# Kernel tuning notes

Hardware: AMD Instinct MI355X
Metric: run time of the kernel (lower is better)

Reference implementation:

```python
import jax, jax.numpy as jnp
import numpy as np

N = 262144   # number of occupied voxels (sparse points)
C = 64       # channels
G = 128
K = 27       # 3x3x3 kernel offsets


def _build_kernel_map(rng):
    # Unique occupied voxel coordinates on a G^3 grid.
    flat = rng.choice(G ** 3, size=N, replace=False)
    order = np.argsort(flat)
    skeys = flat[order]
    coords = np.stack(np.unravel_index(flat, (G, G, G)), axis=1).astype(np.int64)  # [N,3]
    offsets = np.array([[dx, dy, dz] for dx in (-1, 0, 1) for dy in (-1, 0, 1) for dz in (-1, 0, 1)], np.int64)
    nb = np.full((N, K), -1, np.int32)  # -1 == no neighbor at this offset
    for k in range(K):
        nc = coords + offsets[k]
        valid = np.all((nc >= 0) & (nc < G), axis=1)
        nkey = (nc[:, 0] * G + nc[:, 1]) * G + nc[:, 2]
        pos = np.clip(np.searchsorted(skeys, nkey), 0, N - 1)
        hit = valid & (skeys[pos] == nkey)
        nb[hit, k] = order[pos[hit]].astype(np.int32)
    return nb


def setup_inputs() -> dict:
    nb = _build_kernel_map(np.random.default_rng(0))
    key = jax.random.key(0)
    k1, k2, k3, k4, k5 = jax.random.split(key, 5)
    feat = jax.random.normal(k1, (N, C), jnp.float32)
    W = jax.random.normal(k2, (C, C), jnp.float32) / np.float32(np.sqrt(C))   # 1x1 bottleneck weight
    b1 = jax.random.normal(k3, (C,), jnp.float32) * 0.01                      # bottleneck bias
    dw = jax.random.normal(k4, (K, C), jnp.float32) / np.float32(np.sqrt(K))  # channelwise 3^3 kernel
    b2 = jax.random.normal(k5, (C,), jnp.float32) * 0.01                      # channelwise bias
    return {"feat": feat, "neighbor_idx": jnp.asarray(nb), "W": W, "b1": b1, "b2": b2, "dw": dw}


def reference(feat, neighbor_idx, W, b1, b2, dw):
    # bottleneck: 1x1 sparse conv == pointwise linear over features
    bx = feat @ W + b1  # [N,C]
    mask = neighbor_idx >= 0
    safe = jnp.where(mask, neighbor_idx, 0)
    # channelwise (depthwise) 3x3x3 sparse conv: sum over 27 offsets of
    # gathered neighbor features times per-channel weight. scan over the
    # fixed 27 offsets to avoid a [N,27,C] intermediate.
    def body(acc, inp):
        wk, idxk, mk = inp  # [C], [N], [N]
        g = jnp.where(mk[:, None], bx[idxk], 0.0)
        return acc + g * wk, None
    acc, _ = jax.lax.scan(body, jnp.zeros_like(bx), (dw, safe.T, mask.T))
    # residual add (note: the module never applies its ReLU in forward)
    return feat + acc + b2
```

## Files before the change

### kernel.cpp

```cpp
#include <hip/hip_runtime.h>
#include <hip/hip_bf16.h>

#define NPTS 262144
#define NC 64
#define NK 27

typedef __attribute__((ext_vector_type(8))) short bf16x8;
typedef __attribute__((ext_vector_type(4))) float f32x4;

__device__ __forceinline__ unsigned bfr(float x) {
    unsigned u = __float_as_uint(x);
    return (u + 0x7fffu + ((u >> 16) & 1u)) >> 16;
}
__device__ __forceinline__ float bflo(unsigned u) { return __uint_as_float(u << 16); }
__device__ __forceinline__ float bfhi(unsigned u) { return __uint_as_float(u & 0xffff0000u); }

__device__ __forceinline__ unsigned cvtpk(float lo, float hi) {
    unsigned r;
    asm("v_cvt_pk_bf16_f32 %0, %1, %2" : "=v"(r) : "v"(lo), "v"(hi));
    return r;
}

union BF { unsigned u[4]; bf16x8 v; };

__global__ __launch_bounds__(256) void gemm_mfma(const float* __restrict__ feat,
                                                 const float* __restrict__ W,
                                                 const float* __restrict__ b1,
                                                 ushort* __restrict__ bx) {
    __shared__ float Ws[NC * NC];
    __shared__ float b1S[NC];
    int t = threadIdx.x;
#pragma unroll
    for (int i = 0; i < 4; ++i)
        ((float4*)Ws)[t + i * 256] = ((const float4*)W)[t + i * 256];
    if (t < NC) b1S[t] = b1[t];
    __syncthreads();

    int lane = t & 63;
    int col = lane & 15;
    int kg = lane >> 4;
    int wid = blockIdx.x * 4 + (t >> 6);
    const int NWAVES = 1024 * 4;
    const int NTILES = NPTS / 16;

    BF Bf[2][4];
#pragma unroll
    for (int ks = 0; ks < 2; ++ks)
#pragma unroll
        for (int ct = 0; ct < 4; ++ct)
#pragma unroll
            for (int r = 0; r < 4; ++r) {
                float lo = Ws[(ks * 32 + kg * 8 + 2 * r) * NC + ct * 16 + col];
                float hi = Ws[(ks * 32 + kg * 8 + 2 * r + 1) * NC + ct * 16 + col];
                Bf[ks][ct].u[r] = cvtpk(lo, hi);
            }
    float bias[4];
#pragma unroll
    for (int ct = 0; ct < 4; ++ct) bias[ct] = b1S[ct * 16 + col];

    for (int tile = wid; tile < NTILES; tile += NWAVES) {
        long r0 = (long)tile * 16;
        const float* ap = feat + (r0 + col) * NC + kg * 8;
        float4 a0 = *(const float4*)(ap);
        float4 a1 = *(const float4*)(ap + 4);
        float4 a2 = *(const float4*)(ap + 32);
        float4 a3 = *(const float4*)(ap + 36);
        BF A0, A1;
        A0.u[0] = cvtpk(a0.x, a0.y); A0.u[1] = cvtpk(a0.z, a0.w);
        A0.u[2] = cvtpk(a1.x, a1.y); A0.u[3] = cvtpk(a1.z, a1.w);
        A1.u[0] = cvtpk(a2.x, a2.y); A1.u[1] = cvtpk(a2.z, a2.w);
        A1.u[2] = cvtpk(a3.x, a3.y); A1.u[3] = cvtpk(a3.z, a3.w);

        f32x4 acc[4];
#pragma unroll
        for (int ct = 0; ct < 4; ++ct) {
            acc[ct] = (f32x4){bias[ct], bias[ct], bias[ct], bias[ct]};
            acc[ct] = __builtin_amdgcn_mfma_f32_16x16x32_bf16(A0.v, Bf[0][ct].v, acc[ct], 0, 0, 0);
            acc[ct] = __builtin_amdgcn_mfma_f32_16x16x32_bf16(A1.v, Bf[1][ct].v, acc[ct], 0, 0, 0);
        }

        ushort* op = bx + (r0 + kg * 4) * NC + col;
#pragma unroll
        for (int i = 0; i < 4; ++i)
#pragma unroll
            for (int ct = 0; ct < 4; ++ct)
                op[i * NC + ct * 16] = (ushort)bfr(acc[ct][i]);
    }
}

__global__ __launch_bounds__(256) void dwconv(const float* __restrict__ feat,
                                              const int* __restrict__ nb,
                                              const float* __restrict__ b2,
                                              const float* __restrict__ dw,
                                              const ushort* __restrict__ bx,
                                              float* __restrict__ out) {
    __shared__ float dwS[NK * NC];
    __shared__ float b2S[NC];
    int t = threadIdx.x;
    for (int i = t; i < NK * NC; i += 256) dwS[i] = dw[i];
    if (t < NC) b2S[t] = b2[t];
    __syncthreads();

    int b = blockIdx.x;
    int chunk = gridDim.x >> 3;
    int sb = (b & 7) * chunk + (b >> 3);

    long row = (long)sb * 32 + (t >> 3);
    int c0 = (t & 7) * 8;

    const int* nrow = nb + row * NK;
    int idx[NK];
#pragma unroll
    for (int k = 0; k < NK; ++k) idx[k] = nrow[k];

    const float* fp = feat + row * NC + c0;
    float4 fa = *(const float4*)fp;
    float4 fb = *(const float4*)(fp + 4);

    float acc0 = 0.f, acc1 = 0.f, acc2 = 0.f, acc3 = 0.f;
    float acc4 = 0.f, acc5 = 0.f, acc6 = 0.f, acc7 = 0.f;

#pragma unroll
    for (int k = 0; k < NK; ++k) {
        int id = idx[k];
        bool v = id >= 0;
        if (__any(v)) {
            int ids = v ? id : 0;
            uint4 g = *(const uint4*)(bx + (size_t)ids * NC + c0);
            if (!v) { g.x = 0u; g.y = 0u; g.z = 0u; g.w = 0u; }
            float4 w0 = *(const float4*)(dwS + k * NC + c0);
            float4 w1 = *(const float4*)(dwS + k * NC + c0 + 4);
            acc0 += bflo(g.x) * w0.x;
            acc1 += bfhi(g.x) * w0.y;
            acc2 += bflo(g.y) * w0.z;
            acc3 += bfhi(g.y) * w0.w;
            acc4 += bflo(g.z) * w1.x;
            acc5 += bfhi(g.z) * w1.y;
            acc6 += bflo(g.w) * w1.z;
            acc7 += bfhi(g.w) * w1.w;
        }
    }

    float* op = out + row * NC + c0;
    *(float4*)op = make_float4(acc0 + fa.x + b2S[c0 + 0],
                               acc1 + fa.y + b2S[c0 + 1],
                               acc2 + fa.z + b2S[c0 + 2],
                               acc3 + fa.w + b2S[c0 + 3]);
    *(float4*)(op + 4) = make_float4(acc4 + fb.x + b2S[c0 + 4],
                                     acc5 + fb.y + b2S[c0 + 5],
                                     acc6 + fb.z + b2S[c0 + 6],
                                     acc7 + fb.w + b2S[c0 + 7]);
}

extern "C" void kernel_launch(void* const* d_in, const int* in_sizes, int n_in,
                              void* d_out, int out_size, void* d_ws, size_t ws_size,
                              hipStream_t stream) {
    const float* feat = (const float*)d_in[0];
    const int*   nb   = (const int*)d_in[1];
    const float* W    = (const float*)d_in[2];
    const float* b1   = (const float*)d_in[3];
    const float* b2   = (const float*)d_in[4];
    const float* dw   = (const float*)d_in[5];
    float* out = (float*)d_out;
    ushort* bx = (ushort*)d_ws;

    gemm_mfma<<<1024, 256, 0, stream>>>(feat, W, b1, bx);
    dwconv<<<NPTS / 32, 256, 0, stream>>>(feat, nb, b2, dw, bx, out);
}
```

Before: 211.9 us.

## Pack bx stores as bf16 pairs with interleaved channel layout, batch neighbor gathers

The GEMM epilogue now writes bf16 pairs with a single cvt_pk instruction and 32-bit stores, interleaving channel c and c+16 in the bx workspace. The dwconv weights are permuted in shared memory to match this layout, and outputs are de-interleaved. The neighbor-index tile is staged cooperatively into shared memory. Gathers are issued in batches of 9 with the wave-level any-skip removed, so more loads are in flight at once. The cost is higher register pressure.

```diff
diff --git a/kernel.cpp b/kernel.cpp
--- a/kernel.cpp
+++ b/kernel.cpp
@@ -8,10 +8,6 @@
 typedef __attribute__((ext_vector_type(8))) short bf16x8;
 typedef __attribute__((ext_vector_type(4))) float f32x4;
 
-__device__ __forceinline__ unsigned bfr(float x) {
-    unsigned u = __float_as_uint(x);
-    return (u + 0x7fffu + ((u >> 16) & 1u)) >> 16;
-}
 __device__ __forceinline__ float bflo(unsigned u) { return __uint_as_float(u << 16); }
 __device__ __forceinline__ float bfhi(unsigned u) { return __uint_as_float(u & 0xffff0000u); }
 
@@ -22,6 +18,7 @@
 }
 
 union BF { unsigned u[4]; bf16x8 v; };
+
 
 __global__ __launch_bounds__(256) void gemm_mfma(const float* __restrict__ feat,
                                                  const float* __restrict__ W,
@@ -79,12 +76,12 @@
             acc[ct] = __builtin_amdgcn_mfma_f32_16x16x32_bf16(A1.v, Bf[1][ct].v, acc[ct], 0, 0, 0);
         }
 
-        ushort* op = bx + (r0 + kg * 4) * NC + col;
 #pragma unroll
-        for (int i = 0; i < 4; ++i)
-#pragma unroll
-            for (int ct = 0; ct < 4; ++ct)
-                op[i * NC + ct * 16] = (ushort)bfr(acc[ct][i]);
+        for (int i = 0; i < 4; ++i) {
+            uint* bu = (uint*)(bx + (r0 + kg * 4 + i) * NC);
+            bu[col]      = cvtpk(acc[0][i], acc[1][i]);
+            bu[16 + col] = cvtpk(acc[2][i], acc[3][i]);
+        }
     }
 }
 
@@ -96,60 +93,75 @@
                                               float* __restrict__ out) {
     __shared__ float dwS[NK * NC];
     __shared__ float b2S[NC];
+    __shared__ int nbS[32 * NK];
     int t = threadIdx.x;
-    for (int i = t; i < NK * NC; i += 256) dwS[i] = dw[i];
+    for (int i = t; i < NK * NC; i += 256) {
+        int p = i & 63;
+        int ch = ((p >> 1) & 15) + ((p & 1) << 4) + (p & 32);
+        dwS[i] = dw[(i & ~63) + ch];
+    }
     if (t < NC) b2S[t] = b2[t];
-    __syncthreads();
 
     int b = blockIdx.x;
     int chunk = gridDim.x >> 3;
     int sb = (b & 7) * chunk + (b >> 3);
 
-    long row = (long)sb * 32 + (t >> 3);
-    int c0 = (t & 7) * 8;
+    const uint4* nbsrc = (const uint4*)(nb + (size_t)sb * 32 * NK);
+    if (t < 216) ((uint4*)nbS)[t] = nbsrc[t];
+    __syncthreads();
 
-    const int* nrow = nb + row * NK;
-    int idx[NK];
+    int r = t >> 3;
+    int q = t & 7;
+    long row = (long)sb * 32 + r;
+    int lo_c0 = (q < 4) ? 4 * q : 16 + 4 * q;
+    int hi_c0 = lo_c0 + 16;
+
+    float4 flo = *(const float4*)(feat + row * NC + lo_c0);
+    float4 fhi = *(const float4*)(feat + row * NC + hi_c0);
+
+    float acc[8] = {0.f, 0.f, 0.f, 0.f, 0.f, 0.f, 0.f, 0.f};
+
+    const int* nrow = nbS + r * NK;
 #pragma unroll
-    for (int k = 0; k < NK; ++k) idx[k] = nrow[k];
-
-    const float* fp = feat + row * NC + c0;
-    float4 fa = *(const float4*)fp;
-    float4 fb = *(const float4*)(fp + 4);
-
-    float acc0 = 0.f, acc1 = 0.f, acc2 = 0.f, acc3 = 0.f;
-    float acc4 = 0.f, acc5 = 0.f, acc6 = 0.f, acc7 = 0.f;
-
+    for (int batch = 0; batch < 3; ++batch) {
+        int idxv[9];
+        uint4 g[9];
 #pragma unroll
-    for (int k = 0; k < NK; ++k) {
-        int id = idx[k];
-        bool v = id >= 0;
-        if (__any(v)) {
-            int ids = v ? id : 0;
-            uint4 g = *(const uint4*)(bx + (size_t)ids * NC + c0);
-            if (!v) { g.x = 0u; g.y = 0u; g.z = 0u; g.w = 0u; }
-            float4 w0 = *(const float4*)(dwS + k * NC + c0);
-            float4 w1 = *(const float4*)(dwS + k * NC + c0 + 4);
-            acc0 += bflo(g.x) * w0.x;
-            acc1 += bfhi(g.x) * w0.y;
-            acc2 += bflo(g.y) * w0.z;
-            acc3 += bfhi(g.y) * w0.w;
-            acc4 += bflo(g.z) * w1.x;
-            acc5 += bfhi(g.z) * w1.y;
-            acc6 += bflo(g.w) * w1.z;
-            acc7 += bfhi(g.w) * w1.w;
+        for (int j = 0; j < 9; ++j) idxv[j] = nrow[batch * 9 + j];
+#pragma unroll
+        for (int j = 0; j < 9; ++j) {
+            int id = idxv[j];
+            int ids = (id >= 0) ? id : 0;
+            g[j] = *(const uint4*)(bx + (size_t)ids * NC + q * 8);
+        }
+#pragma unroll
+        for (int j = 0; j < 9; ++j) {
+            int k = batch * 9 + j;
+            uint4 gg = g[j];
+            if (idxv[j] < 0) { gg.x = 0u; gg.y = 0u; gg.z = 0u; gg.w = 0u; }
+            float4 w0 = *(const float4*)(dwS + k * NC + q * 8);
+            float4 w1 = *(const float4*)(dwS + k * NC + q * 8 + 4);
+            acc[0] += bflo(gg.x) * w0.x;
+            acc[1] += bfhi(gg.x) * w0.y;
+            acc[2] += bflo(gg.y) * w0.z;
+            acc[3] += bfhi(gg.y) * w0.w;
+            acc[4] += bflo(gg.z) * w1.x;
+            acc[5] += bfhi(gg.z) * w1.y;
+            acc[6] += bflo(gg.w) * w1.z;
+            acc[7] += bfhi(gg.w) * w1.w;
         }
     }
 
-    float* op = out + row * NC + c0;
-    *(float4*)op = make_float4(acc0 + fa.x + b2S[c0 + 0],
-                               acc1 + fa.y + b2S[c0 + 1],
-                               acc2 + fa.z + b2S[c0 + 2],
-                               acc3 + fa.w + b2S[c0 + 3]);
-    *(float4*)(op + 4) = make_float4(acc4 + fb.x + b2S[c0 + 4],
-                                     acc5 + fb.y + b2S[c0 + 5],
-                                     acc6 + fb.z + b2S[c0 + 6],
-                                     acc7 + fb.w + b2S[c0 + 7]);
+    float4 olo = make_float4(acc[0] + flo.x + b2S[lo_c0 + 0],
+                             acc[2] + flo.y + b2S[lo_c0 + 1],
+                             acc[4] + flo.z + b2S[lo_c0 + 2],
+                             acc[6] + flo.w + b2S[lo_c0 + 3]);
+    float4 ohi = make_float4(acc[1] + fhi.x + b2S[hi_c0 + 0],
+                             acc[3] + fhi.y + b2S[hi_c0 + 1],
+                             acc[5] + fhi.z + b2S[hi_c0 + 2],
+                             acc[7] + fhi.w + b2S[hi_c0 + 3]);
+    *(float4*)(out + row * NC + lo_c0) = olo;
+    *(float4*)(out + row * NC + hi_c0) = ohi;
 }
 
 extern "C" void kernel_launch(void* const* d_in, const int* in_sizes, int n_in,
```

Measured after the change: 341.9 us. 1.61x slower.
